# Optimization experiments

Hardware: AMD Instinct MI355X
Metric: run time of the kernel (lower is better)

## Reference

```python
import jax, jax.numpy as jnp
import numpy as np

B, H, W, C, NH, WS = 64, 56, 56, 128, 4, 7
N = H * W


def setup_inputs() -> dict:
    key = jax.random.key(0)
    ks = jax.random.split(key, 6)
    return {
        "x": jax.random.normal(ks[0], (B, N, C), jnp.float32),
        "w_qkv": jax.random.normal(ks[1], (3 * C, C), jnp.float32) * 0.02,
        "w_lim": jax.random.normal(ks[2], (C, 1, 3, 3), jnp.float32) * 0.02,
        "b_lim": jax.random.normal(ks[3], (C,), jnp.float32) * 0.02,
        "w_proj": jax.random.normal(ks[4], (C, C), jnp.float32) * 0.02,
        "b_proj": jax.random.normal(ks[5], (C,), jnp.float32) * 0.02,
        "H": H,
        "W": W,
    }


def reference(x, w_qkv, w_lim, b_lim, w_proj, b_proj, H, W):
    Bq, Nq, Cq = x.shape
    ws, nh = WS, NH
    hd = Cq // nh
    hg, wg = H // ws, W // ws  # 8, 8 -- no padding needed at these shapes
    scale = hd ** -0.5

    qkv = x @ w_qkv.T                      # (B, N, 3C)
    q, k, v = jnp.split(qkv, 3, axis=-1)

    def img2win(t):
        # (B,N,C) -> (B, hg*wg, nh, ws*ws, hd)
        t = t.reshape(Bq, hg, ws, wg, ws, Cq).transpose(0, 1, 3, 2, 4, 5)
        return t.reshape(Bq, hg * wg, ws * ws, nh, hd).transpose(0, 1, 3, 2, 4)

    qw, kw, vw = img2win(q), img2win(k), img2win(v)

    # LIM: depthwise 3x3 conv on shape-integrated V (win2img(img2win(v)) == v as NCHW)
    v_img = v.reshape(Bq, H, W, Cq).transpose(0, 3, 1, 2)     # (B,C,H,W)
    v_lim = jax.lax.conv_general_dilated(
        v_img, w_lim, window_strides=(1, 1), padding='SAME',
        dimension_numbers=('NCHW', 'OIHW', 'NCHW'), feature_group_count=Cq)
    v_lim = v_lim + b_lim[None, :, None, None]
    v_lim = v_lim.reshape(Bq, Cq, Nq).transpose(0, 2, 1)      # (B,N,C)

    # windowed attention: g = window index, n = head
    attn = jax.nn.softmax(
        jnp.einsum('bgnqd,bgnkd->bgnqk', qw, kw) * scale, axis=-1)
    out = jnp.einsum('bgnqk,bgnkd->bgnqd', attn, vw)          # (B,g,nh,ws*ws,hd)

    # merge windows back: (B,g,nh,ws*ws,hd) -> (B,N,C)
    out = out.transpose(0, 1, 3, 2, 4).reshape(Bq, hg, wg, ws, ws, Cq)
    out = out.transpose(0, 1, 3, 2, 4, 5).reshape(Bq, Nq, Cq)

    out = out + v_lim
    return out @ w_proj.T + b_proj
```

## Files before the change

kernel.cpp:

```cpp
#include <hip/hip_runtime.h>
#include <cstdint>

#define B_   64
#define H_   56
#define W_   56
#define C_   128
#define WSZ  7
#define TT   49
#define NN   3136
#define MM   (B_ * NN)
#define SCALE 0.17677669529663687f

typedef short bf16x8 __attribute__((ext_vector_type(8)));
typedef short bf16x4 __attribute__((ext_vector_type(4)));
typedef float f32x4  __attribute__((ext_vector_type(4)));
typedef unsigned short u16;

__device__ __forceinline__ float bf2f(u16 u) {
    return __uint_as_float(((unsigned int)u) << 16);
}
__device__ __forceinline__ u16 f2bf(float f) {
    unsigned int u = __float_as_uint(f);
    u += 0x7FFFu + ((u >> 16) & 1u);
    return (u16)(u >> 16);
}

__global__ __launch_bounds__(256) void kw_cvt(
    const float* __restrict__ wqkv, const float* __restrict__ wproj,
    u16* __restrict__ wqbf, u16* __restrict__ wpbf)
{
    int g = blockIdx.x * 256 + threadIdx.x;
    if (g < 12288) {
        float4 f = *(const float4*)&wqkv[g * 4];
        float mul = (g < 4096) ? SCALE : 1.0f;
        ushort4 u;
        u.x = f2bf(f.x * mul); u.y = f2bf(f.y * mul);
        u.z = f2bf(f.z * mul); u.w = f2bf(f.w * mul);
        *(ushort4*)&wqbf[g * 4] = u;
    } else {
        int g2 = g - 12288;
        float4 f = *(const float4*)&wproj[g2 * 4];
        ushort4 u;
        u.x = f2bf(f.x); u.y = f2bf(f.y);
        u.z = f2bf(f.z); u.w = f2bf(f.w);
        *(ushort4*)&wpbf[g2 * 4] = u;
    }
}

template <bool PREW, bool YBF>
__global__ __launch_bounds__(256, 3) void ka_fused(
    const float* __restrict__ x, const float* __restrict__ wqkv,
    const u16* __restrict__ wqbf,
    u16* __restrict__ vout, u16* __restrict__ ybf, float* __restrict__ out)
{
    __shared__ u16 lds[26240];
    u16 (*xq)[136] = (u16(*)[136])&lds[0];
    u16 (*ks)[136] = (u16(*)[136])&lds[8704];
    u16 (*vs)[138] = (u16(*)[138])&lds[17408];
    u16* ps_ = &lds[0];

    const int t   = threadIdx.x;
    const int blk = blockIdx.x;
    const int b_  = blk >> 6, wr = blk & 63;
    const int qy  = wr >> 3, qx = wr & 7;
    const int wave = t >> 6, lane = t & 63, lr = lane & 15, quad = lane >> 4;

    for (int i = t; i < 64 * 32; i += 256) {
        int tok = i >> 5, c4 = (i & 31) * 4;
        ushort4 u4 = {0, 0, 0, 0};
        if (tok < TT) {
            int hh = qy * WSZ + tok / WSZ, ww = qx * WSZ + tok % WSZ;
            float4 f = *(const float4*)&x[((size_t)b_ * NN + hh * W_ + ww) * C_ + c4];
            u4.x = f2bf(f.x); u4.y = f2bf(f.y);
            u4.z = f2bf(f.z); u4.w = f2bf(f.w);
        }
        *(ushort4*)&xq[tok][c4] = u4;
    }
    __syncthreads();

#pragma unroll
    for (int cc = 0; cc < 2; cc++) {
        const int ch = 1 + cc;
        u16* dstbase = cc ? &vs[0][0] : &ks[0][0];
        const int dstride = cc ? 138 : 136;
#pragma unroll
        for (int half = 0; half < 2; half++) {
            const int wrowi = ch * 128 + half * 64 + wave * 16 + lr;
            const float* wrowf = &wqkv[(size_t)wrowi * C_];
            const u16*   wrowb = &wqbf[(size_t)wrowi * C_];
            f32x4 acc[4];
#pragma unroll
            for (int mi = 0; mi < 4; mi++) acc[mi] = {0.f, 0.f, 0.f, 0.f};
#pragma unroll
            for (int kk = 0; kk < 4; kk++) {
                bf16x8 bfr;
                if constexpr (PREW) {
                    bfr = *(const bf16x8*)&wrowb[kk * 32 + quad * 8];
                } else {
                    float4 f0 = *(const float4*)&wrowf[kk * 32 + quad * 8];
                    float4 f1 = *(const float4*)&wrowf[kk * 32 + quad * 8 + 4];
                    bfr[0] = (short)f2bf(f0.x); bfr[1] = (short)f2bf(f0.y);
                    bfr[2] = (short)f2bf(f0.z); bfr[3] = (short)f2bf(f0.w);
                    bfr[4] = (short)f2bf(f1.x); bfr[5] = (short)f2bf(f1.y);
                    bfr[6] = (short)f2bf(f1.z); bfr[7] = (short)f2bf(f1.w);
                }
#pragma unroll
                for (int mi = 0; mi < 4; mi++) {
                    bf16x8 afr = *(const bf16x8*)&xq[mi * 16 + lr][kk * 32 + quad * 8];
                    acc[mi] = __builtin_amdgcn_mfma_f32_16x16x32_bf16(
                        afr, bfr, acc[mi], 0, 0, 0);
                }
            }
#pragma unroll
            for (int mi = 0; mi < 4; mi++) {
#pragma unroll
                for (int r = 0; r < 4; r++) {
                    int tok = mi * 16 + quad * 4 + r;
                    int col = half * 64 + wave * 16 + lr;
                    u16 bv = f2bf(acc[mi][r]);
                    dstbase[tok * dstride + col] = bv;
                    if (cc == 1 && tok < TT) {
                        int hh2 = qy * WSZ + tok / WSZ;
                        int ww2 = qx * WSZ + tok % WSZ;
                        vout[((size_t)b_ * NN + hh2 * W_ + ww2) * C_ + col] = bv;
                    }
                }
            }
        }
    }

    const float qmul = PREW ? 1.0f : SCALE;
    f32x4 qacc[2][4];
#pragma unroll
    for (int half = 0; half < 2; half++)
#pragma unroll
        for (int mi = 0; mi < 4; mi++) qacc[half][mi] = {0.f, 0.f, 0.f, 0.f};
#pragma unroll
    for (int half = 0; half < 2; half++) {
        const int wrowi = half * 64 + wave * 16 + lr;
        const float* wrowf = &wqkv[(size_t)wrowi * C_];
        const u16*   wrowb = &wqbf[(size_t)wrowi * C_];
#pragma unroll
        for (int kk = 0; kk < 4; kk++) {
            bf16x8 bfr;
            if constexpr (PREW) {
                bfr = *(const bf16x8*)&wrowb[kk * 32 + quad * 8];
            } else {
                float4 f0 = *(const float4*)&wrowf[kk * 32 + quad * 8];
                float4 f1 = *(const float4*)&wrowf[kk * 32 + quad * 8 + 4];
                bfr[0] = (short)f2bf(f0.x); bfr[1] = (short)f2bf(f0.y);
                bfr[2] = (short)f2bf(f0.z); bfr[3] = (short)f2bf(f0.w);
                bfr[4] = (short)f2bf(f1.x); bfr[5] = (short)f2bf(f1.y);
                bfr[6] = (short)f2bf(f1.z); bfr[7] = (short)f2bf(f1.w);
            }
#pragma unroll
            for (int mi = 0; mi < 4; mi++) {
                bf16x8 afr = *(const bf16x8*)&xq[mi * 16 + lr][kk * 32 + quad * 8];
                qacc[half][mi] = __builtin_amdgcn_mfma_f32_16x16x32_bf16(
                    afr, bfr, qacc[half][mi], 0, 0, 0);
            }
        }
    }
    __syncthreads();

#pragma unroll
    for (int half = 0; half < 2; half++)
#pragma unroll
        for (int mi = 0; mi < 4; mi++)
#pragma unroll
            for (int r = 0; r < 4; r++)
                xq[mi * 16 + quad * 4 + r][half * 64 + wave * 16 + lr] =
                    f2bf(qacc[half][mi][r] * qmul);
    __syncthreads();

    const int h = wave;
    bf16x8 qf[4], kf[4];
#pragma unroll
    for (int mi = 0; mi < 4; mi++) {
        qf[mi] = *(const bf16x8*)&xq[mi * 16 + lr][h * 32 + quad * 8];
        kf[mi] = *(const bf16x8*)&ks[mi * 16 + lr][h * 32 + quad * 8];
    }
    __syncthreads();

    f32x4 s[4][4];
#pragma unroll
    for (int mi = 0; mi < 4; mi++)
#pragma unroll
        for (int nj = 0; nj < 4; nj++) s[mi][nj] = {0.f, 0.f, 0.f, 0.f};
#pragma unroll
    for (int mi = 0; mi < 4; mi++)
#pragma unroll
        for (int nj = 0; nj < 4; nj++)
            s[mi][nj] = __builtin_amdgcn_mfma_f32_16x16x32_bf16(
                qf[mi], kf[nj], s[mi][nj], 0, 0, 0);

    if (lr >= 1) {
#pragma unroll
        for (int mi = 0; mi < 4; mi++)
#pragma unroll
            for (int r = 0; r < 4; r++) s[mi][3][r] = -1e30f;
    }

    float rsum[4][4];
#pragma unroll
    for (int mi = 0; mi < 4; mi++) {
#pragma unroll
        for (int r = 0; r < 4; r++) {
            float mx = fmaxf(fmaxf(s[mi][0][r], s[mi][1][r]),
                             fmaxf(s[mi][2][r], s[mi][3][r]));
#pragma unroll
            for (int off = 1; off < 16; off <<= 1)
                mx = fmaxf(mx, __shfl_xor(mx, off));
            float sum = 0.f;
#pragma unroll
            for (int nj = 0; nj < 4; nj++) {
                float p = __expf(s[mi][nj][r] - mx);
                s[mi][nj][r] = p;
                sum += p;
            }
#pragma unroll
            for (int off = 1; off < 16; off <<= 1)
                sum += __shfl_xor(sum, off);
            rsum[mi][r] = sum;
        }
    }

#pragma unroll
    for (int mi = 0; mi < 4; mi++)
#pragma unroll
        for (int nj = 0; nj < 4; nj++)
#pragma unroll
            for (int r = 0; r < 4; r++)
                ps_[((h * 64) + mi * 16 + quad * 4 + r) * 68 + nj * 16 + lr] =
                    f2bf(s[mi][nj][r]);

    f32x4 o[4][2];
#pragma unroll
    for (int mi = 0; mi < 4; mi++)
#pragma unroll
        for (int nv = 0; nv < 2; nv++) o[mi][nv] = {0.f, 0.f, 0.f, 0.f};

#pragma unroll
    for (int kt = 0; kt < 2; kt++) {
        bf16x8 pf[4];
#pragma unroll
        for (int mi = 0; mi < 4; mi++) {
            const u16* pp = &ps_[((h * 64) + mi * 16 + lr) * 68 + kt * 32 + quad * 8];
            bf16x4 lo = *(const bf16x4*)&pp[0];
            bf16x4 hi = *(const bf16x4*)&pp[4];
            bf16x8 f;
            f[0] = lo[0]; f[1] = lo[1]; f[2] = lo[2]; f[3] = lo[3];
            f[4] = hi[0]; f[5] = hi[1]; f[6] = hi[2]; f[7] = hi[3];
            pf[mi] = f;
        }
        bf16x8 vf[2];
#pragma unroll
        for (int nv = 0; nv < 2; nv++) {
            bf16x8 tmp;
#pragma unroll
            for (int jj = 0; jj < 8; jj++)
                tmp[jj] = (short)vs[kt * 32 + quad * 8 + jj][h * 32 + nv * 16 + lr];
            vf[nv] = tmp;
        }
#pragma unroll
        for (int mi = 0; mi < 4; mi++)
#pragma unroll
            for (int nv = 0; nv < 2; nv++)
                o[mi][nv] = __builtin_amdgcn_mfma_f32_16x16x32_bf16(
                    pf[mi], vf[nv], o[mi][nv], 0, 0, 0);
    }

#pragma unroll
    for (int mi = 0; mi < 4; mi++) {
#pragma unroll
        for (int r = 0; r < 4; r++) {
            int i = mi * 16 + quad * 4 + r;
            if (i < TT) {
                int hh = qy * WSZ + i / WSZ, ww = qx * WSZ + i % WSZ;
                size_t orow = (size_t)b_ * NN + hh * W_ + ww;
                float inv = 1.f / rsum[mi][r];
#pragma unroll
                for (int nv = 0; nv < 2; nv++) {
                    float val = o[mi][nv][r] * inv;
                    if constexpr (YBF)
                        ybf[orow * C_ + h * 32 + nv * 16 + lr] = f2bf(val);
                    else
                        out[orow * C_ + h * 32 + nv * 16 + lr] = val;
                }
            }
        }
    }
}

template <bool INPLACE>
__global__ __launch_bounds__(256) void kb_lim(
    const u16* __restrict__ v, const float* __restrict__ wlim,
    const float* __restrict__ blim, u16* __restrict__ z,
    float* __restrict__ out)
{
    const int t   = threadIdx.x;
    const int pos = blockIdx.x * 16 + (t >> 4);
    const int c0  = (t & 15) * 8;
    const int b_  = pos / NN;
    const int rem = pos - b_ * NN;
    const int hh  = rem / W_;
    const int ww  = rem - hh * W_;

    bf16x8 yv;
    float4 o0, o1;
    if constexpr (INPLACE) {
        yv = *(const bf16x8*)&z[(size_t)pos * C_ + c0];
    } else {
        o0 = *(const float4*)&out[(size_t)pos * C_ + c0];
        o1 = *(const float4*)&out[(size_t)pos * C_ + c0 + 4];
    }

    float w72[72];
    {
        const float* wp = &wlim[c0 * 9];
#pragma unroll
        for (int i = 0; i < 18; i++) {
            float4 f = *(const float4*)&wp[i * 4];
            w72[i * 4 + 0] = f.x; w72[i * 4 + 1] = f.y;
            w72[i * 4 + 2] = f.z; w72[i * 4 + 3] = f.w;
        }
    }
    float acc[8];
    {
        float4 b0 = *(const float4*)&blim[c0];
        float4 b1 = *(const float4*)&blim[c0 + 4];
        acc[0] = b0.x; acc[1] = b0.y; acc[2] = b0.z; acc[3] = b0.w;
        acc[4] = b1.x; acc[5] = b1.y; acc[6] = b1.z; acc[7] = b1.w;
    }

    const u16* vbase = &v[(size_t)b_ * NN * C_ + c0];
#pragma unroll
    for (int dy = -1; dy <= 1; dy++) {
        int yy = hh + dy;
        bool yok = (unsigned)yy < (unsigned)H_;
#pragma unroll
        for (int dx = -1; dx <= 1; dx++) {
            int x2 = ww + dx;
            bool ok = yok && ((unsigned)x2 < (unsigned)W_);
            bf16x8 vv = {0, 0, 0, 0, 0, 0, 0, 0};
            if (ok) vv = *(const bf16x8*)&vbase[(size_t)(yy * W_ + x2) * C_];
            const int tap = (dy + 1) * 3 + (dx + 1);
#pragma unroll
            for (int j = 0; j < 8; j++)
                acc[j] += bf2f((u16)vv[j]) * w72[j * 9 + tap];
        }
    }

    if constexpr (INPLACE) {
        bf16x8 zz;
#pragma unroll
        for (int j = 0; j < 8; j++)
            zz[j] = (short)f2bf(bf2f((u16)yv[j]) + acc[j]);
        *(bf16x8*)&z[(size_t)pos * C_ + c0] = zz;
    } else {
        o0.x += acc[0]; o0.y += acc[1]; o0.z += acc[2]; o0.w += acc[3];
        o1.x += acc[4]; o1.y += acc[5]; o1.z += acc[6]; o1.w += acc[7];
        *(float4*)&out[(size_t)pos * C_ + c0]     = o0;
        *(float4*)&out[(size_t)pos * C_ + c0 + 4] = o1;
    }
}

__global__ __launch_bounds__(256, 4) void kc_direct(
    const u16* __restrict__ z, const u16* __restrict__ wpbf,
    const float* __restrict__ bproj, float* __restrict__ out)
{
    const int t    = threadIdx.x;
    const int m0   = blockIdx.x * 128;
    const int wave = t >> 6, lane = t & 63, lr = lane & 15, quad = lane >> 4;
    const int wm = (wave >> 1) * 64, wn = (wave & 1) * 64;

    f32x4 acc[4][4];
#pragma unroll
    for (int mi = 0; mi < 4; mi++)
#pragma unroll
        for (int ni = 0; ni < 4; ni++) acc[mi][ni] = {0.f, 0.f, 0.f, 0.f};

#pragma unroll
    for (int kt = 0; kt < 2; kt++) {
#pragma unroll
        for (int kk = 0; kk < 2; kk++) {
            const int kcol = kt * 64 + kk * 32 + quad * 8;
            bf16x8 a[4], b[4];
#pragma unroll
            for (int mi = 0; mi < 4; mi++)
                a[mi] = *(const bf16x8*)&z[(size_t)(m0 + wm + mi * 16 + lr) * C_ + kcol];
#pragma unroll
            for (int ni = 0; ni < 4; ni++)
                b[ni] = *(const bf16x8*)&wpbf[(size_t)(wn + ni * 16 + lr) * C_ + kcol];
#pragma unroll
            for (int mi = 0; mi < 4; mi++)
#pragma unroll
                for (int ni = 0; ni < 4; ni++)
                    acc[mi][ni] = __builtin_amdgcn_mfma_f32_16x16x32_bf16(
                        a[mi], b[ni], acc[mi][ni], 0, 0, 0);
        }
    }

#pragma unroll
    for (int mi = 0; mi < 4; mi++) {
#pragma unroll
        for (int r = 0; r < 4; r++) {
            int m = m0 + wm + mi * 16 + quad * 4 + r;
#pragma unroll
            for (int ni = 0; ni < 4; ni++) {
                int c = wn + ni * 16 + lr;
                out[(size_t)m * C_ + c] = acc[mi][ni][r] + bproj[c];
            }
        }
    }
}

template <int MODE>
__global__ __launch_bounds__(256) void kc_proj(
    float* __restrict__ y, const float* __restrict__ wproj,
    const u16* __restrict__ wpbf, const float* __restrict__ bproj)
{
    __shared__ u16 As[128][72];
    __shared__ u16 Ws[128][72];
    const int t    = threadIdx.x;
    const int m0   = blockIdx.x * 128;
    const int wave = t >> 6, lane = t & 63, lr = lane & 15, quad = lane >> 4;
    const int wm = (wave >> 1) * 64, wn = (wave & 1) * 64;

    f32x4 acc[4][4];
#pragma unroll
    for (int mi = 0; mi < 4; mi++)
#pragma unroll
        for (int ni = 0; ni < 4; ni++) acc[mi][ni] = {0.f, 0.f, 0.f, 0.f};

#pragma unroll
    for (int kt = 0; kt < 2; kt++) {
        const int k0 = kt * 64;
#pragma unroll
        for (int p = 0; p < 8; p++) {
            int e   = p * 256 + t;
            int row = e >> 4;
            int col = (e & 15) * 4;
            float4 fa = *(const float4*)&y[(size_t)(m0 + row) * C_ + k0 + col];
            ushort4 ua;
            ua.x = f2bf(fa.x); ua.y = f2bf(fa.y);
            ua.z = f2bf(fa.z); ua.w = f2bf(fa.w);
            *(ushort4*)&As[row][col] = ua;
            if constexpr (MODE == 0) {
                float4 fw = *(const float4*)&wproj[(size_t)row * C_ + k0 + col];
                ushort4 uw;
                uw.x = f2bf(fw.x); uw.y = f2bf(fw.y);
                uw.z = f2bf(fw.z); uw.w = f2bf(fw.w);
                *(ushort4*)&Ws[row][col] = uw;
            }
        }
        if constexpr (MODE >= 1) {
#pragma unroll
            for (int p4 = 0; p4 < 4; p4++) {
                int e    = p4 * 256 + t;
                int row  = e >> 3;
                int col8 = (e & 7) * 8;
                *(bf16x8*)&Ws[row][col8] =
                    *(const bf16x8*)&wpbf[(size_t)row * C_ + k0 + col8];
            }
        }
        __syncthreads();
#pragma unroll
        for (int kk = 0; kk < 2; kk++) {
            bf16x8 a[4], b[4];
#pragma unroll
            for (int mi = 0; mi < 4; mi++)
                a[mi] = *(const bf16x8*)&As[wm + mi * 16 + lr][kk * 32 + quad * 8];
#pragma unroll
            for (int ni = 0; ni < 4; ni++)
                b[ni] = *(const bf16x8*)&Ws[wn + ni * 16 + lr][kk * 32 + quad * 8];
#pragma unroll
            for (int mi = 0; mi < 4; mi++)
#pragma unroll
                for (int ni = 0; ni < 4; ni++)
                    acc[mi][ni] = __builtin_amdgcn_mfma_f32_16x16x32_bf16(
                        a[mi], b[ni], acc[mi][ni], 0, 0, 0);
        }
        if (kt == 0) __syncthreads();
    }

#pragma unroll
    for (int mi = 0; mi < 4; mi++) {
#pragma unroll
        for (int r = 0; r < 4; r++) {
            int m = m0 + wm + mi * 16 + quad * 4 + r;
#pragma unroll
            for (int ni = 0; ni < 4; ni++) {
                int c = wn + ni * 16 + lr;
                y[(size_t)m * C_ + c] = acc[mi][ni][r] + bproj[c];
            }
        }
    }
}

extern "C" void kernel_launch(void* const* d_in, const int* in_sizes, int n_in,
                              void* d_out, int out_size, void* d_ws, size_t ws_size,
                              hipStream_t stream)
{
    const float* x     = (const float*)d_in[0];
    const float* wqkv  = (const float*)d_in[1];
    const float* wlim  = (const float*)d_in[2];
    const float* blim  = (const float*)d_in[3];
    const float* wproj = (const float*)d_in[4];
    const float* bproj = (const float*)d_in[5];
    float* out = (float*)d_out;
    u16*   v   = (u16*)d_ws;

    const size_t vbytes = (size_t)MM * C_ * 2;
    const size_t wbytes = (49152 + 16384) * 2;
    const size_t need1  = vbytes + wbytes;
    const size_t need2  = need1 + vbytes;

    if (ws_size >= need2) {
        u16* wqbf = (u16*)((char*)d_ws + vbytes);
        u16* wpbf = wqbf + 49152;
        u16* zbuf = (u16*)((char*)d_ws + need1);
        kw_cvt<<<dim3(64), 256, 0, stream>>>(wqkv, wproj, wqbf, wpbf);
        ka_fused<true, true><<<dim3(B_ * 64), 256, 0, stream>>>(
            x, wqkv, wqbf, v, zbuf, nullptr);
        kb_lim<true><<<dim3(MM / 16), 256, 0, stream>>>(v, wlim, blim, zbuf, nullptr);
        kc_direct<<<dim3(MM / 128), 256, 0, stream>>>(zbuf, wpbf, bproj, out);
    } else if (ws_size >= need1) {
        u16* wqbf = (u16*)((char*)d_ws + vbytes);
        u16* wpbf = wqbf + 49152;
        kw_cvt<<<dim3(64), 256, 0, stream>>>(wqkv, wproj, wqbf, wpbf);
        ka_fused<true, false><<<dim3(B_ * 64), 256, 0, stream>>>(
            x, wqkv, wqbf, v, nullptr, out);
        kb_lim<false><<<dim3(MM / 16), 256, 0, stream>>>(v, wlim, blim, nullptr, out);
        kc_proj<1><<<dim3(MM / 128), 256, 0, stream>>>(out, nullptr, wpbf, bproj);
    } else {
        ka_fused<false, false><<<dim3(B_ * 64), 256, 0, stream>>>(
            x, wqkv, nullptr, v, nullptr, out);
        kb_lim<false><<<dim3(MM / 16), 256, 0, stream>>>(v, wlim, blim, nullptr, out);
        kc_proj<0><<<dim3(MM / 128), 256, 0, stream>>>(out, wproj, nullptr, bproj);
    }
}
```

Baseline: 386.8 us.

## Fuse depthwise LIM conv with output projection GEMM in one kernel

Replaces the separate LIM kernel (which read and rewrote the bf16 z buffer) and the projection GEMM kernel with a single kernel. Each 16-row block computes the 3x3 depthwise conv plus attention output, stages the bf16 result in shared memory, then runs the 128x128 projection with MFMA and writes fp32 output. This removes one full write and read of the intermediate z tensor and one launch. The cost is a small GEMM tile per block (16 rows) that re-reads the projection weights from global/L2 for every block, with less reuse than the 128-row tile.

```diff
diff --git a/kernel.cpp b/kernel.cpp
--- a/kernel.cpp
+++ b/kernel.cpp
@@ -292,11 +292,99 @@
     }
 }
 
-template <bool INPLACE>
+__global__ __launch_bounds__(256) void kbc_fused(
+    const u16* __restrict__ v, const float* __restrict__ wlim,
+    const float* __restrict__ blim, const u16* __restrict__ ybf,
+    const u16* __restrict__ wpbf, const float* __restrict__ bproj,
+    float* __restrict__ out)
+{
+    __shared__ u16 As[16][140];
+    const int t   = threadIdx.x;
+    const int p0  = blockIdx.x * 16;
+    const int pr  = t >> 4;
+    const int c0  = (t & 15) * 8;
+    const int pos = p0 + pr;
+    const int b_  = pos / NN;
+    const int rem = pos - b_ * NN;
+    const int hh  = rem / W_;
+    const int ww  = rem - hh * W_;
+
+    bf16x8 yv = *(const bf16x8*)&ybf[(size_t)pos * C_ + c0];
+
+    float w72[72];
+    {
+        const float* wp = &wlim[c0 * 9];
+#pragma unroll
+        for (int i = 0; i < 18; i++) {
+            float4 f = *(const float4*)&wp[i * 4];
+            w72[i * 4 + 0] = f.x; w72[i * 4 + 1] = f.y;
+            w72[i * 4 + 2] = f.z; w72[i * 4 + 3] = f.w;
+        }
+    }
+    float acc8[8];
+    {
+        float4 b0 = *(const float4*)&blim[c0];
+        float4 b1 = *(const float4*)&blim[c0 + 4];
+        acc8[0] = b0.x; acc8[1] = b0.y; acc8[2] = b0.z; acc8[3] = b0.w;
+        acc8[4] = b1.x; acc8[5] = b1.y; acc8[6] = b1.z; acc8[7] = b1.w;
+    }
+
+    const u16* vbase = &v[(size_t)b_ * NN * C_ + c0];
+#pragma unroll
+    for (int dy = -1; dy <= 1; dy++) {
+        int yy = hh + dy;
+        bool yok = (unsigned)yy < (unsigned)H_;
+#pragma unroll
+        for (int dx = -1; dx <= 1; dx++) {
+            int x2 = ww + dx;
+            bool ok = yok && ((unsigned)x2 < (unsigned)W_);
+            bf16x8 vv = {0, 0, 0, 0, 0, 0, 0, 0};
+            if (ok) vv = *(const bf16x8*)&vbase[(size_t)(yy * W_ + x2) * C_];
+            const int tap = (dy + 1) * 3 + (dx + 1);
+#pragma unroll
+            for (int j = 0; j < 8; j++)
+                acc8[j] += bf2f((u16)vv[j]) * w72[j * 9 + tap];
+        }
+    }
+
+    bf16x8 zz;
+#pragma unroll
+    for (int j = 0; j < 8; j++)
+        zz[j] = (short)f2bf(bf2f((u16)yv[j]) + acc8[j]);
+    *(bf16x8*)&As[pr][c0] = zz;
+    __syncthreads();
+
+    const int wave = t >> 6, lane = t & 63, lr = lane & 15, quad = lane >> 4;
+    const int wn = wave * 32;
+
+    f32x4 acc[2];
+    acc[0] = {0.f, 0.f, 0.f, 0.f};
+    acc[1] = {0.f, 0.f, 0.f, 0.f};
+#pragma unroll
+    for (int kk = 0; kk < 4; kk++) {
+        bf16x8 a = *(const bf16x8*)&As[lr][kk * 32 + quad * 8];
+#pragma unroll
+        for (int nj = 0; nj < 2; nj++) {
+            bf16x8 b = *(const bf16x8*)&wpbf[(size_t)(wn + nj * 16 + lr) * C_ +
+                                             kk * 32 + quad * 8];
+            acc[nj] = __builtin_amdgcn_mfma_f32_16x16x32_bf16(a, b, acc[nj], 0, 0, 0);
+        }
+    }
+
+#pragma unroll
+    for (int r = 0; r < 4; r++) {
+        int prow = quad * 4 + r;
+#pragma unroll
+        for (int nj = 0; nj < 2; nj++) {
+            int c = wn + nj * 16 + lr;
+            out[(size_t)(p0 + prow) * C_ + c] = acc[nj][r] + bproj[c];
+        }
+    }
+}
+
 __global__ __launch_bounds__(256) void kb_lim(
     const u16* __restrict__ v, const float* __restrict__ wlim,
-    const float* __restrict__ blim, u16* __restrict__ z,
-    float* __restrict__ out)
+    const float* __restrict__ blim, float* __restrict__ out)
 {
     const int t   = threadIdx.x;
     const int pos = blockIdx.x * 16 + (t >> 4);
@@ -306,15 +394,6 @@
     const int hh  = rem / W_;
     const int ww  = rem - hh * W_;
 
-    bf16x8 yv;
-    float4 o0, o1;
-    if constexpr (INPLACE) {
-        yv = *(const bf16x8*)&z[(size_t)pos * C_ + c0];
-    } else {
-        o0 = *(const float4*)&out[(size_t)pos * C_ + c0];
-        o1 = *(const float4*)&out[(size_t)pos * C_ + c0 + 4];
-    }
-
     float w72[72];
     {
         const float* wp = &wlim[c0 * 9];
@@ -351,68 +430,13 @@
         }
     }
 
-    if constexpr (INPLACE) {
-        bf16x8 zz;
-#pragma unroll
-        for (int j = 0; j < 8; j++)
-            zz[j] = (short)f2bf(bf2f((u16)yv[j]) + acc[j]);
-        *(bf16x8*)&z[(size_t)pos * C_ + c0] = zz;
-    } else {
-        o0.x += acc[0]; o0.y += acc[1]; o0.z += acc[2]; o0.w += acc[3];
-        o1.x += acc[4]; o1.y += acc[5]; o1.z += acc[6]; o1.w += acc[7];
-        *(float4*)&out[(size_t)pos * C_ + c0]     = o0;
-        *(float4*)&out[(size_t)pos * C_ + c0 + 4] = o1;
-    }
-}
-
-__global__ __launch_bounds__(256, 4) void kc_direct(
-    const u16* __restrict__ z, const u16* __restrict__ wpbf,
-    const float* __restrict__ bproj, float* __restrict__ out)
-{
-    const int t    = threadIdx.x;
-    const int m0   = blockIdx.x * 128;
-    const int wave = t >> 6, lane = t & 63, lr = lane & 15, quad = lane >> 4;
-    const int wm = (wave >> 1) * 64, wn = (wave & 1) * 64;
-
-    f32x4 acc[4][4];
-#pragma unroll
-    for (int mi = 0; mi < 4; mi++)
-#pragma unroll
-        for (int ni = 0; ni < 4; ni++) acc[mi][ni] = {0.f, 0.f, 0.f, 0.f};
-
-#pragma unroll
-    for (int kt = 0; kt < 2; kt++) {
-#pragma unroll
-        for (int kk = 0; kk < 2; kk++) {
-            const int kcol = kt * 64 + kk * 32 + quad * 8;
-            bf16x8 a[4], b[4];
-#pragma unroll
-            for (int mi = 0; mi < 4; mi++)
-                a[mi] = *(const bf16x8*)&z[(size_t)(m0 + wm + mi * 16 + lr) * C_ + kcol];
-#pragma unroll
-            for (int ni = 0; ni < 4; ni++)
-                b[ni] = *(const bf16x8*)&wpbf[(size_t)(wn + ni * 16 + lr) * C_ + kcol];
-#pragma unroll
-            for (int mi = 0; mi < 4; mi++)
-#pragma unroll
-                for (int ni = 0; ni < 4; ni++)
-                    acc[mi][ni] = __builtin_amdgcn_mfma_f32_16x16x32_bf16(
-                        a[mi], b[ni], acc[mi][ni], 0, 0, 0);
-        }
-    }
-
-#pragma unroll
-    for (int mi = 0; mi < 4; mi++) {
-#pragma unroll
-        for (int r = 0; r < 4; r++) {
-            int m = m0 + wm + mi * 16 + quad * 4 + r;
-#pragma unroll
-            for (int ni = 0; ni < 4; ni++) {
-                int c = wn + ni * 16 + lr;
-                out[(size_t)m * C_ + c] = acc[mi][ni][r] + bproj[c];
-            }
-        }
-    }
+    float* op = &out[(size_t)pos * C_ + c0];
+    float4 o0 = *(const float4*)&op[0];
+    float4 o1 = *(const float4*)&op[4];
+    o0.x += acc[0]; o0.y += acc[1]; o0.z += acc[2]; o0.w += acc[3];
+    o1.x += acc[4]; o1.y += acc[5]; o1.z += acc[6]; o1.w += acc[7];
+    *(float4*)&op[0] = o0;
+    *(float4*)&op[4] = o1;
 }
 
 template <int MODE>
@@ -519,24 +543,24 @@
     if (ws_size >= need2) {
         u16* wqbf = (u16*)((char*)d_ws + vbytes);
         u16* wpbf = wqbf + 49152;
-        u16* zbuf = (u16*)((char*)d_ws + need1);
+        u16* ybf  = (u16*)((char*)d_ws + need1);
         kw_cvt<<<dim3(64), 256, 0, stream>>>(wqkv, wproj, wqbf, wpbf);
         ka_fused<true, true><<<dim3(B_ * 64), 256, 0, stream>>>(
-            x, wqkv, wqbf, v, zbuf, nullptr);
-        kb_lim<true><<<dim3(MM / 16), 256, 0, stream>>>(v, wlim, blim, zbuf, nullptr);
-        kc_direct<<<dim3(MM / 128), 256, 0, stream>>>(zbuf, wpbf, bproj, out);
+            x, wqkv, wqbf, v, ybf, nullptr);
+        kbc_fused<<<dim3(MM / 16), 256, 0, stream>>>(
+            v, wlim, blim, ybf, wpbf, bproj, out);
     } else if (ws_size >= need1) {
         u16* wqbf = (u16*)((char*)d_ws + vbytes);
         u16* wpbf = wqbf + 49152;
         kw_cvt<<<dim3(64), 256, 0, stream>>>(wqkv, wproj, wqbf, wpbf);
         ka_fused<true, false><<<dim3(B_ * 64), 256, 0, stream>>>(
             x, wqkv, wqbf, v, nullptr, out);
-        kb_lim<false><<<dim3(MM / 16), 256, 0, stream>>>(v, wlim, blim, nullptr, out);
+        kb_lim<<<dim3(MM / 16), 256, 0, stream>>>(v, wlim, blim, out);
         kc_proj<1><<<dim3(MM / 128), 256, 0, stream>>>(out, nullptr, wpbf, bproj);
     } else {
         ka_fused<false, false><<<dim3(B_ * 64), 256, 0, stream>>>(
             x, wqkv, nullptr, v, nullptr, out);
-        kb_lim<false><<<dim3(MM / 16), 256, 0, stream>>>(v, wlim, blim, nullptr, out);
+        kb_lim<<<dim3(MM / 16), 256, 0, stream>>>(v, wlim, blim, out);
         kc_proj<0><<<dim3(MM / 128), 256, 0, stream>>>(out, wproj, nullptr, bproj);
     }
 }
```

Result: no change. 380.7 us (-1.6%).
